# Kernel tuning notes

Measured on AMD Instinct MI355X. Metric: run time of the kernel, lower is better.

Reference implementation:

```python
import jax, jax.numpy as jnp
import numpy as np

B, C, CI, H, W = 4, 256, 128, 64, 64  # batch, in_channels, inter_channels, spatial


def conv1x1(x, w, b):
    # x: [B,C,H,W], w: [O,C], b: [O] -> [B,O,H,W]
    return jnp.einsum('bchw,oc->bohw', x, w) + b[None, :, None, None]


def setup_inputs() -> dict:
    key = jax.random.key(0)
    ks = jax.random.split(key, 9)
    s = 0.02
    return {
        'x':  jax.random.normal(ks[0], (B, C, H, W), dtype=jnp.float32),
        'Wg': jax.random.normal(ks[1], (CI, C), dtype=jnp.float32) * s,
        'bg': jnp.zeros((CI,), dtype=jnp.float32),
        'Wt': jax.random.normal(ks[2], (CI, C), dtype=jnp.float32) * s,
        'bt': jnp.zeros((CI,), dtype=jnp.float32),
        'Wp': jax.random.normal(ks[3], (CI, C), dtype=jnp.float32) * s,
        'bp': jnp.zeros((CI,), dtype=jnp.float32),
        'Wo': jax.random.normal(ks[4], (C, CI), dtype=jnp.float32) * s,
        'bo': jnp.zeros((C,), dtype=jnp.float32),
    }


def reference(x, Wg, bg, Wt, bt, Wp, bp, Wo, bo):
    b, c, h, w = x.shape
    n = h * w
    g  = conv1x1(x, Wg, bg).reshape(b, -1, n)   # [B,CI,N]
    th = conv1x1(x, Wt, bt).reshape(b, -1, n)   # [B,CI,N]
    ph = conv1x1(x, Wp, bp).reshape(b, -1, n)   # [B,CI,N]
    f = jnp.einsum('bci,bcj->bij', th, ph)      # [B,N,N] unscaled scores
    a = jax.nn.softmax(f, axis=-1)
    y = jnp.einsum('bij,bcj->bci', a, g)        # [B,CI,N]
    y = y.reshape(b, -1, h, w)
    return conv1x1(y, Wo, bo) + x
```

## Files before the change

### kernel.cpp

```cpp
#include <hip/hip_runtime.h>
#include <math.h>

#define B_  4
#define C_  256
#define CI_ 128
#define N_  4096

typedef short s16x8  __attribute__((ext_vector_type(8)));
typedef float f32x4  __attribute__((ext_vector_type(4)));
typedef float f32x16 __attribute__((ext_vector_type(16)));

__device__ inline ushort f2bf(float f) {
    unsigned int u = __float_as_uint(f);
    u += 0x7FFF + ((u >> 16) & 1);
    return (ushort)(u >> 16);
}
__device__ inline float bf2f(ushort u) {
    return __uint_as_float(((unsigned int)u) << 16);
}

__device__ inline unsigned pkbf(float a, float b) {
    unsigned r;
    asm("v_cvt_pk_bf16_f32 %0, %1, %2" : "=v"(r) : "v"(a), "v"(b));
    return r;
}
__device__ inline void plswap(unsigned &x, unsigned &y) {
    asm volatile("v_permlane32_swap_b32 %0, %1" : "+v"(x), "+v"(y));
}

__device__ inline void gload_lds16(const void* g, void* l) {
    __builtin_amdgcn_global_load_lds(
        (const __attribute__((address_space(1))) unsigned int*)g,
        (__attribute__((address_space(3))) unsigned int*)l, 16, 0, 0);
}

__device__ inline void block_sync_lds() {
    asm volatile("s_waitcnt lgkmcnt(0)" ::: "memory");
    __builtin_amdgcn_s_barrier();
    asm volatile("" ::: "memory");
}

__global__ __launch_bounds__(256) void prep_kernel(
    const float* __restrict__ Wg, const float* __restrict__ Wt,
    const float* __restrict__ Wp, const float* __restrict__ Wo,
    const float* __restrict__ bg, const float* __restrict__ bt,
    const float* __restrict__ bp,
    ushort* __restrict__ Wcat, ushort* __restrict__ Wobf,
    float* __restrict__ bcat,
    const float* __restrict__ x, ushort* __restrict__ xT)
{
    __shared__ ushort Ls[64][72];
    const int bid = blockIdx.x;
    const int t = threadIdx.x;
    if (bid < 512) {
        int i = bid * 256 + t;
        if (i < 32768)       Wcat[i] = f2bf(Wg[i]);
        else if (i < 65536)  Wcat[i] = f2bf(Wt[i - 32768]);
        else if (i < 98304)  Wcat[i] = f2bf(Wp[i - 65536]);
        else if (i < 131072) Wobf[i - 98304] = f2bf(Wo[i - 98304]);
        if (i < 128)         bcat[i] = bg[i];
        else if (i < 256)    bcat[i] = bt[i - 128];
        else if (i < 384)    bcat[i] = bp[i - 256];
        return;
    }
    int idx2 = bid - 512;
    const int n0 = (idx2 & 63) * 64;
    const int c0 = ((idx2 >> 6) & 3) * 64;
    const int b  = idx2 >> 8;
    const float* xb = x + ((size_t)b * C_ + c0) * N_ + n0;
    #pragma unroll
    for (int r = 0; r < 4; r++) {
        int idx = t + 256 * r;
        int c = idx >> 4, n4 = (idx & 15) * 4;
        float4 v = *(const float4*)&xb[(size_t)c * N_ + n4];
        ushort4 o;
        o.x = f2bf(v.x); o.y = f2bf(v.y); o.z = f2bf(v.z); o.w = f2bf(v.w);
        *(ushort4*)&Ls[c][n4] = o;
    }
    __syncthreads();
    ushort* xTb = xT + ((size_t)b * N_ + n0) * C_ + c0;
    #pragma unroll
    for (int r = 0; r < 2; r++) {
        int idx = t + 256 * r;
        int n = idx >> 3, c8 = (idx & 7) * 8;
        ushort tmp[8];
        #pragma unroll
        for (int u = 0; u < 8; u++) tmp[u] = Ls[c8 + u][n];
        *(uint4*)&xTb[(size_t)n * C_ + c8] = *(uint4*)tmp;
    }
}

__global__ __launch_bounds__(256) void proj_kernel(
    const ushort* __restrict__ Wcat, const float* __restrict__ bcat,
    const ushort* __restrict__ xT,
    ushort* __restrict__ g, ushort* __restrict__ tht, ushort* __restrict__ pht)
{
    __shared__ ushort Ws[192][72];
    __shared__ ushort Xs[64][72];
    const int b = blockIdx.z, yy = blockIdx.y, n0 = blockIdx.x * 64;
    const int t = threadIdx.x, wv = t >> 6, lane = t & 63;
    const int g4 = lane >> 4, ln = lane & 15;
    const ushort* Xsrc = xT + ((size_t)b * N_ + n0) * C_;

    f32x4 accg[4], acct[2][4];
    #pragma unroll
    for (int i = 0; i < 4; i++) {
        accg[i] = (f32x4){0.f, 0.f, 0.f, 0.f};
        acct[0][i] = (f32x4){0.f, 0.f, 0.f, 0.f};
        acct[1][i] = (f32x4){0.f, 0.f, 0.f, 0.f};
    }

    for (int k0 = 0; k0 < C_; k0 += 64) {
        block_sync_lds();
        #pragma unroll
        for (int r = 0; r < 6; r++) {
            int idx = t + 256 * r;
            int row = idx >> 3, k8 = (idx & 7) * 8;
            int srow = ((row >> 6) * 2 + yy) * 64 + (row & 63);
            *(uint4*)&Ws[row][k8] = *(const uint4*)&Wcat[(size_t)srow * C_ + k0 + k8];
        }
        #pragma unroll
        for (int r = 0; r < 2; r++) {
            int idx = t + 256 * r;
            int row = idx >> 3, k8 = (idx & 7) * 8;
            *(uint4*)&Xs[row][k8] = *(const uint4*)&Xsrc[(size_t)row * C_ + k0 + k8];
        }
        block_sync_lds();
        #pragma unroll
        for (int kk = 0; kk < 2; kk++) {
            s16x8 aW = *(const s16x8*)&Ws[16 * wv + ln][32 * kk + 8 * g4];
            #pragma unroll
            for (int nt = 0; nt < 4; nt++) {
                s16x8 bX = *(const s16x8*)&Xs[16 * nt + ln][32 * kk + 8 * g4];
                accg[nt] = __builtin_amdgcn_mfma_f32_16x16x32_bf16(aW, bX, accg[nt], 0, 0, 0);
            }
            s16x8 aX = *(const s16x8*)&Xs[16 * wv + ln][32 * kk + 8 * g4];
            #pragma unroll
            for (int mi = 0; mi < 2; mi++) {
                #pragma unroll
                for (int ct = 0; ct < 4; ct++) {
                    s16x8 bW = *(const s16x8*)&Ws[64 + 64 * mi + 16 * ct + ln][32 * kk + 8 * g4];
                    acct[mi][ct] = __builtin_amdgcn_mfma_f32_16x16x32_bf16(aX, bW, acct[mi][ct], 0, 0, 0);
                }
            }
        }
    }

    {
        ushort* ob = g + (size_t)b * CI_ * N_;
        #pragma unroll
        for (int r = 0; r < 4; r++) {
            int mloc = 16 * wv + 4 * g4 + r;
            float bi = bcat[yy * 64 + mloc];
            #pragma unroll
            for (int nt = 0; nt < 4; nt++)
                ob[(size_t)(yy * 64 + mloc) * N_ + n0 + 16 * nt + ln] = f2bf(accg[nt][r] + bi);
        }
    }
    #pragma unroll
    for (int mi = 0; mi < 2; mi++) {
        int mt = 2 + 2 * mi + yy;
        ushort* ob = (mi == 0 ? tht : pht) + (size_t)b * N_ * CI_;
        int cib = yy * 64;
        #pragma unroll
        for (int r = 0; r < 4; r++) {
            int nloc = 16 * wv + 4 * g4 + r;
            #pragma unroll
            for (int ct = 0; ct < 4; ct++) {
                float bi = bcat[mt * 64 + 16 * ct + ln];
                ob[(size_t)(n0 + nloc) * CI_ + cib + 16 * ct + ln] = f2bf(acct[mi][ct][r] + bi);
            }
        }
    }
}


__device__ inline float build_pa(const f32x16& S, s16x8& f0, s16x8& f1) {
    unsigned w[8];
    #pragma unroll
    for (int e = 0; e < 8; e++)
        w[e] = pkbf(__expf(S[2 * e]), __expf(S[2 * e + 1]));
    float ls = 0.f;
    #pragma unroll
    for (int e = 0; e < 8; e++)
        ls += __uint_as_float(w[e] << 16) + __uint_as_float(w[e] & 0xFFFF0000u);
    plswap(w[0], w[2]);
    plswap(w[1], w[3]);
    plswap(w[4], w[6]);
    plswap(w[5], w[7]);
    union { unsigned u[4]; s16x8 v; } A, B;
    A.u[0] = w[0]; A.u[1] = w[1]; A.u[2] = w[2]; A.u[3] = w[3];
    B.u[0] = w[4]; B.u[1] = w[5]; B.u[2] = w[6]; B.u[3] = w[7];
    f0 = A.v; f1 = B.v;
    return ls;
}

#define STAGE_KV(bufofs, jsrc) do {                                          \
    _Pragma("unroll")                                                        \
    for (int r_ = 0; r_ < 4; r_++) {                                         \
        int c_   = (wv << 2) + r_;                                           \
        int row_ = (c_ << 2) + kr;                                           \
        int src_ = (((jsrc) + row_) << 8) + (kc ^ ((row_ & 7) << 4));        \
        gload_lds16(kB + src_, smemB + (bufofs) + (c_ << 10));               \
    }                                                                        \
    _Pragma("unroll")                                                        \
    for (int r_ = 0; r_ < 4; r_++) {                                         \
        int c_   = (wv << 2) + r_;                                           \
        int row_ = (c_ << 3) + vr;                                           \
        int src_ = row_ * (N_ * 2) + ((jsrc) << 1) + (vc ^ ((row_ & 7) << 4));\
        gload_lds16(vB + src_, smemB + (bufofs) + 16384 + (c_ << 10));       \
    }                                                                        \
} while (0)

#define NC_ 4
#define JC_ (N_ / NC_)

__global__ __launch_bounds__(256, 2) void attn_mfma_kernel(
    const ushort* __restrict__ qn,
    const ushort* __restrict__ kn,
    const ushort* __restrict__ vm,
    ushort* __restrict__ Opart,
    float* __restrict__ lbuf)
{
    __shared__ __align__(16) char smemB[65536];

    constexpr int NI = N_ / 128;
    constexpr int nb = NI * NC_ * B_;
    int flat = (blockIdx.z * NC_ + blockIdx.y) * NI + blockIdx.x;
    int nf   = (flat & 7) * (nb / 8) + (flat >> 3);
    const int i0    = (nf % NI) * 128;
    const int chunk = (nf / NI) % NC_;
    const int b     = nf / (NI * NC_);
    const int jbase = chunk * JC_;

    const int t    = threadIdx.x;
    const int wv   = t >> 6;
    const int lane = t & 63;
    const int n32  = lane & 31;
    const int h    = lane >> 5;
    const int swz  = (n32 & 7) << 4;

    const char* kB = (const char*)(kn + (size_t)b * N_ * CI_);
    const char* vB = (const char*)(vm + (size_t)b * CI_ * N_);

    const ushort* qb = qn + ((size_t)b * N_ + i0) * CI_;
    s16x8 aQ[8];
    #pragma unroll
    for (int kk = 0; kk < 8; kk++)
        aQ[kk] = *(const s16x8*)(qb + (size_t)(32 * wv + n32) * CI_ + 16 * kk + 8 * h);

    f32x16 Oacc[4];
    #pragma unroll
    for (int dt = 0; dt < 4; dt++)
        #pragma unroll
        for (int e = 0; e < 16; e++) Oacc[dt][e] = 0.f;
    float lsum = 0.f;

    const int kr = lane >> 4;
    const int kc = (lane & 15) << 4;
    const int vr = lane >> 3;
    const int vc = (lane & 7) << 4;

    STAGE_KV(0, jbase);
    int buf = 0;
    for (int jt = jbase; jt < jbase + JC_; jt += 64) {
        if (jt + 64 < jbase + JC_) {
            STAGE_KV(buf ^ 32768, jt + 64);
            asm volatile("s_waitcnt vmcnt(8)" ::: "memory");
        } else {
            asm volatile("s_waitcnt vmcnt(0)" ::: "memory");
        }
        __builtin_amdgcn_s_barrier();
        asm volatile("" ::: "memory");

        const char* Kc = smemB + buf;
        const char* Vc = smemB + buf + 16384;

        s16x8 pa[4];
        {
            f32x16 S0;
            #pragma unroll
            for (int e = 0; e < 16; e++) S0[e] = 0.f;
            __builtin_amdgcn_s_setprio(1);
            #pragma unroll
            for (int kk = 0; kk < 8; kk++) {
                s16x8 aK = *(const s16x8*)(Kc + (n32 << 8) + (((kk << 5) + (h << 4)) ^ swz));
                S0 = __builtin_amdgcn_mfma_f32_32x32x16_bf16(aK, aQ[kk], S0, 0, 0, 0);
            }
            __builtin_amdgcn_s_setprio(0);
            lsum += build_pa(S0, pa[0], pa[1]);
        }
        {
            f32x16 S1;
            #pragma unroll
            for (int e = 0; e < 16; e++) S1[e] = 0.f;
            __builtin_amdgcn_s_setprio(1);
            #pragma unroll
            for (int kk = 0; kk < 8; kk++) {
                s16x8 aK = *(const s16x8*)(Kc + 8192 + (n32 << 8) + (((kk << 5) + (h << 4)) ^ swz));
                S1 = __builtin_amdgcn_mfma_f32_32x32x16_bf16(aK, aQ[kk], S1, 0, 0, 0);
            }
            __builtin_amdgcn_s_setprio(0);
            lsum += build_pa(S1, pa[2], pa[3]);
        }

        __builtin_amdgcn_s_setprio(1);
        #pragma unroll
        for (int dt = 0; dt < 4; dt++) {
            #pragma unroll
            for (int kk = 0; kk < 4; kk++) {
                s16x8 bV = *(const s16x8*)(Vc + ((32 * dt + n32) << 7)
                                              + (((kk << 5) + (h << 4)) ^ swz));
                Oacc[dt] = __builtin_amdgcn_mfma_f32_32x32x16_bf16(pa[kk], bV, Oacc[dt], 0, 0, 0);
            }
        }
        __builtin_amdgcn_s_setprio(0);

        block_sync_lds();
        buf ^= 32768;
    }

    ushort* Ob = Opart + (size_t)chunk * (B_ * N_ * CI_) + ((size_t)b * N_ + i0) * CI_;
    #pragma unroll
    for (int rg = 0; rg < 16; rg++) {
        int R = (rg & 3) + 8 * (rg >> 2) + 4 * h;
        int q = 32 * wv + R;
        #pragma unroll
        for (int dt = 0; dt < 4; dt++)
            Ob[(size_t)q * CI_ + 32 * dt + n32] = f2bf(Oacc[dt][rg]);
    }
    float ot  = __shfl_xor(lsum, 32);
    float tot = lsum + ot;
    if (h == 0)
        lbuf[((size_t)chunk * B_ + b) * N_ + i0 + 32 * wv + n32] = tot;
}

__global__ __launch_bounds__(256) void outgemm_kernel(
    const ushort* __restrict__ Wobf, const float* __restrict__ bo,
    const ushort* __restrict__ Opart, const float* __restrict__ lbuf,
    const float* __restrict__ x, float* __restrict__ out)
{
    __shared__ ushort Ws[64][72];
    __shared__ ushort Ys[64][72];
    const int b = blockIdx.z, m0 = blockIdx.y * 64, n0 = blockIdx.x * 64;
    const int t = threadIdx.x, wv = t >> 6, lane = t & 63;
    const int g4 = lane >> 4, ln = lane & 15;
    const ushort* Wsrc = Wobf + (size_t)m0 * CI_;
    const size_t cs = (size_t)B_ * N_ * CI_;

    f32x4 acc[4];
    #pragma unroll
    for (int i = 0; i < 4; i++) acc[i] = (f32x4){0.f, 0.f, 0.f, 0.f};

    for (int k0 = 0; k0 < CI_; k0 += 64) {
        block_sync_lds();
        #pragma unroll
        for (int r = 0; r < 2; r++) {
            int idx = t + 256 * r;
            int row = idx >> 3, k8 = (idx & 7) * 8;
            *(uint4*)&Ws[row][k8] = *(const uint4*)&Wsrc[(size_t)row * CI_ + k0 + k8];
            size_t obase = ((size_t)b * N_ + n0 + row) * CI_ + k0 + k8;
            float lsum = 0.f;
            #pragma unroll
            for (int c = 0; c < NC_; c++)
                lsum += lbuf[((size_t)c * B_ + b) * N_ + n0 + row];
            float inv = 1.0f / lsum;
            float osum[8];
            #pragma unroll
            for (int u = 0; u < 8; u++) osum[u] = 0.f;
            #pragma unroll
            for (int c = 0; c < NC_; c++) {
                ushort oc[8];
                *(uint4*)oc = *(const uint4*)&Opart[(size_t)c * cs + obase];
                #pragma unroll
                for (int u = 0; u < 8; u++) osum[u] += bf2f(oc[u]);
            }
            ushort yo[8];
            #pragma unroll
            for (int u = 0; u < 8; u++) yo[u] = f2bf(osum[u] * inv);
            *(uint4*)&Ys[row][k8] = *(uint4*)yo;
        }
        block_sync_lds();
        #pragma unroll
        for (int kk = 0; kk < 2; kk++) {
            s16x8 aW = *(const s16x8*)&Ws[16 * wv + ln][32 * kk + 8 * g4];
            #pragma unroll
            for (int nt = 0; nt < 4; nt++) {
                s16x8 bY = *(const s16x8*)&Ys[16 * nt + ln][32 * kk + 8 * g4];
                acc[nt] = __builtin_amdgcn_mfma_f32_16x16x32_bf16(aW, bY, acc[nt], 0, 0, 0);
            }
        }
    }

    float* outb = out + (size_t)b * C_ * N_;
    const float* xb = x + (size_t)b * C_ * N_;
    #pragma unroll
    for (int r = 0; r < 4; r++) {
        int m = m0 + 16 * wv + 4 * g4 + r;
        float bi = bo[m];
        #pragma unroll
        for (int nt = 0; nt < 4; nt++) {
            size_t idx = (size_t)m * N_ + n0 + 16 * nt + ln;
            outb[idx] = acc[nt][r] + bi + xb[idx];
        }
    }
}

extern "C" void kernel_launch(void* const* d_in, const int* in_sizes, int n_in,
                              void* d_out, int out_size, void* d_ws, size_t ws_size,
                              hipStream_t stream) {
    const float* x  = (const float*)d_in[0];
    const float* Wg = (const float*)d_in[1];
    const float* bg = (const float*)d_in[2];
    const float* Wt = (const float*)d_in[3];
    const float* bt = (const float*)d_in[4];
    const float* Wp = (const float*)d_in[5];
    const float* bp = (const float*)d_in[6];
    const float* Wo = (const float*)d_in[7];
    const float* bo = (const float*)d_in[8];
    float* out = (float*)d_out;

    char* w = (char*)d_ws;
    ushort* xT    = (ushort*)w;
    ushort* Opart = (ushort*)w;
    ushort* g     = (ushort*)(w + 16777216);
    ushort* tht   = (ushort*)(w + 20971520);
    ushort* pht   = (ushort*)(w + 25165824);
    ushort* Wcat  = (ushort*)(w + 29360128);
    ushort* Wobf  = (ushort*)(w + 29556736);
    float*  bcat  = (float*) (w + 29622272);
    float*  lbuf  = (float*) (w + 29623808);

    dim3 blk(256);
    prep_kernel<<<1536, blk, 0, stream>>>(Wg, Wt, Wp, Wo, bg, bt, bp,
                                          Wcat, Wobf, bcat, x, xT);
    proj_kernel<<<dim3(N_ / 64, 2, B_), blk, 0, stream>>>(Wcat, bcat, xT, g, tht, pht);
    attn_mfma_kernel<<<dim3(N_ / 128, NC_, B_), blk, 0, stream>>>(tht, pht, g, Opart, lbuf);
    outgemm_kernel<<<dim3(N_ / 64, C_ / 64, B_), blk, 0, stream>>>(Wobf, bo, Opart, lbuf, x, out);
}
```

Baseline: 150.9 us.

## Retile projection and output GEMMs to 128x128 with async LDS loads

Rewrites the projection and output 1x1-conv GEMMs to use 128x128 block tiles with 2x2 wave layout and 4x4 MFMA accumulators per wave. Operands are staged through global-to-LDS direct loads into XOR-swizzled shared memory, double-buffered in the projection kernel. The output kernel computes the softmax normalisers once per tile in shared memory. This aims to raise operand reuse and cut LDS bank conflicts and load latency, at the cost of more registers, more shared memory per block and fewer blocks in the grid.

```diff
diff --git a/kernel.cpp b/kernel.cpp
--- a/kernel.cpp
+++ b/kernel.cpp
@@ -90,90 +90,117 @@
     }
 }
 
-__global__ __launch_bounds__(256) void proj_kernel(
+__global__ __launch_bounds__(256, 2) void proj_kernel(
     const ushort* __restrict__ Wcat, const float* __restrict__ bcat,
     const ushort* __restrict__ xT,
     ushort* __restrict__ g, ushort* __restrict__ tht, ushort* __restrict__ pht)
 {
-    __shared__ ushort Ws[192][72];
-    __shared__ ushort Xs[64][72];
-    const int b = blockIdx.z, yy = blockIdx.y, n0 = blockIdx.x * 64;
+    __shared__ __align__(16) char smem[65536];
+    const int b = blockIdx.z, mt = blockIdx.y, n0 = blockIdx.x * 128;
     const int t = threadIdx.x, wv = t >> 6, lane = t & 63;
+    const int wr = wv >> 1, wc = wv & 1;
     const int g4 = lane >> 4, ln = lane & 15;
-    const ushort* Xsrc = xT + ((size_t)b * N_ + n0) * C_;
-
-    f32x4 accg[4], acct[2][4];
-    #pragma unroll
-    for (int i = 0; i < 4; i++) {
-        accg[i] = (f32x4){0.f, 0.f, 0.f, 0.f};
-        acct[0][i] = (f32x4){0.f, 0.f, 0.f, 0.f};
-        acct[1][i] = (f32x4){0.f, 0.f, 0.f, 0.f};
-    }
-
-    for (int k0 = 0; k0 < C_; k0 += 64) {
+
+    const char* Asrc = (const char*)(Wcat + (size_t)mt * 128 * C_);
+    const char* Bsrc = (const char*)(xT + ((size_t)b * N_ + n0) * C_);
+
+    const int sr = lane >> 3;
+    const int sc = (lane & 7) << 4;
+    const int ssw = sc ^ (sr << 4);
+
+    f32x4 acc[4][4];
+    #pragma unroll
+    for (int i = 0; i < 4; i++)
+        #pragma unroll
+        for (int j = 0; j < 4; j++) acc[i][j] = (f32x4){0.f, 0.f, 0.f, 0.f};
+
+    const int rsw = (ln & 7) << 4;
+
+#define PROJ_STAGE(bufofs, k0) do {                                          \
+    _Pragma("unroll")                                                        \
+    for (int r_ = 0; r_ < 4; r_++) {                                         \
+        int c_   = (wv << 2) + r_;                                           \
+        int row_ = (c_ << 3) + sr;                                           \
+        gload_lds16(Asrc + (size_t)row_ * 512 + (k0) * 2 + ssw,              \
+                    smem + (bufofs) + (c_ << 10));                           \
+        gload_lds16(Bsrc + (size_t)row_ * 512 + (k0) * 2 + ssw,              \
+                    smem + (bufofs) + 16384 + (c_ << 10));                   \
+    }                                                                        \
+} while (0)
+
+    PROJ_STAGE(0, 0);
+    int buf = 0;
+    #pragma unroll
+    for (int s = 0; s < 4; s++) {
+        if (s < 3) {
+            PROJ_STAGE(buf ^ 32768, (s + 1) * 64);
+            asm volatile("s_waitcnt vmcnt(8)" ::: "memory");
+        } else {
+            asm volatile("s_waitcnt vmcnt(0)" ::: "memory");
+        }
+        __builtin_amdgcn_s_barrier();
+        asm volatile("" ::: "memory");
+
+        const char* Ab = smem + buf;
+        const char* Bb = smem + buf + 16384;
+        #pragma unroll
+        for (int kk = 0; kk < 2; kk++) {
+            s16x8 aW[4], bX[4];
+            #pragma unroll
+            for (int m4 = 0; m4 < 4; m4++)
+                aW[m4] = *(const s16x8*)(Ab + ((wr * 64 + m4 * 16 + ln) << 7)
+                                            + (((kk << 6) + (g4 << 4)) ^ rsw));
+            #pragma unroll
+            for (int nt = 0; nt < 4; nt++)
+                bX[nt] = *(const s16x8*)(Bb + ((wc * 64 + nt * 16 + ln) << 7)
+                                            + (((kk << 6) + (g4 << 4)) ^ rsw));
+            __builtin_amdgcn_s_setprio(1);
+            #pragma unroll
+            for (int m4 = 0; m4 < 4; m4++)
+                #pragma unroll
+                for (int nt = 0; nt < 4; nt++)
+                    acc[m4][nt] = __builtin_amdgcn_mfma_f32_16x16x32_bf16(
+                        aW[m4], bX[nt], acc[m4][nt], 0, 0, 0);
+            __builtin_amdgcn_s_setprio(0);
+        }
         block_sync_lds();
-        #pragma unroll
-        for (int r = 0; r < 6; r++) {
-            int idx = t + 256 * r;
-            int row = idx >> 3, k8 = (idx & 7) * 8;
-            int srow = ((row >> 6) * 2 + yy) * 64 + (row & 63);
-            *(uint4*)&Ws[row][k8] = *(const uint4*)&Wcat[(size_t)srow * C_ + k0 + k8];
-        }
-        #pragma unroll
-        for (int r = 0; r < 2; r++) {
-            int idx = t + 256 * r;
-            int row = idx >> 3, k8 = (idx & 7) * 8;
-            *(uint4*)&Xs[row][k8] = *(const uint4*)&Xsrc[(size_t)row * C_ + k0 + k8];
-        }
-        block_sync_lds();
-        #pragma unroll
-        for (int kk = 0; kk < 2; kk++) {
-            s16x8 aW = *(const s16x8*)&Ws[16 * wv + ln][32 * kk + 8 * g4];
+        buf ^= 32768;
+    }
+
+    if (mt == 0) {
+        ushort* ob = g + (size_t)b * CI_ * N_;
+        #pragma unroll
+        for (int m4 = 0; m4 < 4; m4++) {
+            #pragma unroll
+            for (int r = 0; r < 4; r++) {
+                int m = wr * 64 + m4 * 16 + 4 * g4 + r;
+                float bi = bcat[m];
+                #pragma unroll
+                for (int nt = 0; nt < 4; nt++) {
+                    int n = n0 + wc * 64 + nt * 16 + ln;
+                    ob[(size_t)m * N_ + n] = f2bf(acc[m4][nt][r] + bi);
+                }
+            }
+        }
+    } else {
+        ushort* ob = (mt == 1 ? tht : pht) + (size_t)b * N_ * CI_;
+        const float* bb = bcat + mt * 128;
+        #pragma unroll
+        for (int m4 = 0; m4 < 4; m4++) {
+            int mbase = wr * 64 + m4 * 16 + 4 * g4;
             #pragma unroll
             for (int nt = 0; nt < 4; nt++) {
-                s16x8 bX = *(const s16x8*)&Xs[16 * nt + ln][32 * kk + 8 * g4];
-                accg[nt] = __builtin_amdgcn_mfma_f32_16x16x32_bf16(aW, bX, accg[nt], 0, 0, 0);
-            }
-            s16x8 aX = *(const s16x8*)&Xs[16 * wv + ln][32 * kk + 8 * g4];
-            #pragma unroll
-            for (int mi = 0; mi < 2; mi++) {
+                int n = n0 + wc * 64 + nt * 16 + ln;
+                ushort v4[4];
                 #pragma unroll
-                for (int ct = 0; ct < 4; ct++) {
-                    s16x8 bW = *(const s16x8*)&Ws[64 + 64 * mi + 16 * ct + ln][32 * kk + 8 * g4];
-                    acct[mi][ct] = __builtin_amdgcn_mfma_f32_16x16x32_bf16(aX, bW, acct[mi][ct], 0, 0, 0);
-                }
-            }
-        }
-    }
-
-    {
-        ushort* ob = g + (size_t)b * CI_ * N_;
-        #pragma unroll
-        for (int r = 0; r < 4; r++) {
-            int mloc = 16 * wv + 4 * g4 + r;
-            float bi = bcat[yy * 64 + mloc];
-            #pragma unroll
-            for (int nt = 0; nt < 4; nt++)
-                ob[(size_t)(yy * 64 + mloc) * N_ + n0 + 16 * nt + ln] = f2bf(accg[nt][r] + bi);
-        }
-    }
-    #pragma unroll
-    for (int mi = 0; mi < 2; mi++) {
-        int mt = 2 + 2 * mi + yy;
-        ushort* ob = (mi == 0 ? tht : pht) + (size_t)b * N_ * CI_;
-        int cib = yy * 64;
-        #pragma unroll
-        for (int r = 0; r < 4; r++) {
-            int nloc = 16 * wv + 4 * g4 + r;
-            #pragma unroll
-            for (int ct = 0; ct < 4; ct++) {
-                float bi = bcat[mt * 64 + 16 * ct + ln];
-                ob[(size_t)(n0 + nloc) * CI_ + cib + 16 * ct + ln] = f2bf(acct[mi][ct][r] + bi);
-            }
-        }
-    }
-}
-
+                for (int r = 0; r < 4; r++)
+                    v4[r] = f2bf(acc[m4][nt][r] + bb[mbase + r]);
+                *(ushort4*)&ob[(size_t)n * CI_ + mbase] = *(ushort4*)v4;
+            }
+        }
+    }
+#undef PROJ_STAGE
+}
 
 __device__ inline float build_pa(const f32x16& S, s16x8& f0, s16x8& f1) {
     unsigned w[8];
@@ -335,73 +362,109 @@
         lbuf[((size_t)chunk * B_ + b) * N_ + i0 + 32 * wv + n32] = tot;
 }
 
-__global__ __launch_bounds__(256) void outgemm_kernel(
+__global__ __launch_bounds__(256, 2) void outgemm_kernel(
     const ushort* __restrict__ Wobf, const float* __restrict__ bo,
     const ushort* __restrict__ Opart, const float* __restrict__ lbuf,
     const float* __restrict__ x, float* __restrict__ out)
 {
-    __shared__ ushort Ws[64][72];
-    __shared__ ushort Ys[64][72];
-    const int b = blockIdx.z, m0 = blockIdx.y * 64, n0 = blockIdx.x * 64;
+    __shared__ __align__(16) char smem[65536];
+    __shared__ float invL[128];
+    const int b = blockIdx.z, m0 = blockIdx.y * 128, n0 = blockIdx.x * 128;
     const int t = threadIdx.x, wv = t >> 6, lane = t & 63;
+    const int wr = wv >> 1, wc = wv & 1;
     const int g4 = lane >> 4, ln = lane & 15;
-    const ushort* Wsrc = Wobf + (size_t)m0 * CI_;
     const size_t cs = (size_t)B_ * N_ * CI_;
 
-    f32x4 acc[4];
-    #pragma unroll
-    for (int i = 0; i < 4; i++) acc[i] = (f32x4){0.f, 0.f, 0.f, 0.f};
-
-    for (int k0 = 0; k0 < CI_; k0 += 64) {
-        block_sync_lds();
-        #pragma unroll
-        for (int r = 0; r < 2; r++) {
-            int idx = t + 256 * r;
-            int row = idx >> 3, k8 = (idx & 7) * 8;
-            *(uint4*)&Ws[row][k8] = *(const uint4*)&Wsrc[(size_t)row * CI_ + k0 + k8];
-            size_t obase = ((size_t)b * N_ + n0 + row) * CI_ + k0 + k8;
-            float lsum = 0.f;
-            #pragma unroll
-            for (int c = 0; c < NC_; c++)
-                lsum += lbuf[((size_t)c * B_ + b) * N_ + n0 + row];
-            float inv = 1.0f / lsum;
+    {
+        const char* Wsrc = (const char*)(Wobf + (size_t)m0 * CI_);
+        int srl = lane >> 4;
+        int scl = (lane & 15) << 4;
+        #pragma unroll
+        for (int r = 0; r < 8; r++) {
+            int c   = (wv << 3) + r;
+            int row = (c << 2) + srl;
+            gload_lds16(Wsrc + (size_t)row * 256 + (scl ^ ((row & 15) << 4)),
+                        smem + (c << 10));
+        }
+    }
+
+    if (t < 128) {
+        float ls = 0.f;
+        #pragma unroll
+        for (int c = 0; c < NC_; c++)
+            ls += lbuf[((size_t)c * B_ + b) * N_ + n0 + t];
+        invL[t] = 1.0f / ls;
+    }
+    block_sync_lds();
+
+    {
+        #pragma unroll
+        for (int r = 0; r < 8; r++) {
+            int c   = t + 256 * r;
+            int row = c >> 4;
+            int col = (c & 15) << 4;
+            size_t obase = ((size_t)b * N_ + n0 + row) * CI_ + (c & 15) * 8;
+            float inv = invL[row];
             float osum[8];
             #pragma unroll
             for (int u = 0; u < 8; u++) osum[u] = 0.f;
             #pragma unroll
-            for (int c = 0; c < NC_; c++) {
+            for (int cc = 0; cc < NC_; cc++) {
                 ushort oc[8];
-                *(uint4*)oc = *(const uint4*)&Opart[(size_t)c * cs + obase];
+                *(uint4*)oc = *(const uint4*)&Opart[(size_t)cc * cs + obase];
                 #pragma unroll
                 for (int u = 0; u < 8; u++) osum[u] += bf2f(oc[u]);
             }
             ushort yo[8];
             #pragma unroll
             for (int u = 0; u < 8; u++) yo[u] = f2bf(osum[u] * inv);
-            *(uint4*)&Ys[row][k8] = *(uint4*)yo;
-        }
-        block_sync_lds();
-        #pragma unroll
-        for (int kk = 0; kk < 2; kk++) {
-            s16x8 aW = *(const s16x8*)&Ws[16 * wv + ln][32 * kk + 8 * g4];
-            #pragma unroll
-            for (int nt = 0; nt < 4; nt++) {
-                s16x8 bY = *(const s16x8*)&Ys[16 * nt + ln][32 * kk + 8 * g4];
-                acc[nt] = __builtin_amdgcn_mfma_f32_16x16x32_bf16(aW, bY, acc[nt], 0, 0, 0);
-            }
-        }
+            *(uint4*)(smem + 32768 + row * 256 + (col ^ ((row & 15) << 4))) = *(uint4*)yo;
+        }
+    }
+    asm volatile("s_waitcnt vmcnt(0)" ::: "memory");
+    block_sync_lds();
+
+    f32x4 acc[4][4];
+    #pragma unroll
+    for (int i = 0; i < 4; i++)
+        #pragma unroll
+        for (int j = 0; j < 4; j++) acc[i][j] = (f32x4){0.f, 0.f, 0.f, 0.f};
+
+    const int rsw = ln << 4;
+    #pragma unroll
+    for (int kk = 0; kk < 4; kk++) {
+        s16x8 aW[4], bY[4];
+        #pragma unroll
+        for (int m4 = 0; m4 < 4; m4++)
+            aW[m4] = *(const s16x8*)(smem + ((wr * 64 + m4 * 16 + ln) << 8)
+                                          + (((kk << 6) + (g4 << 4)) ^ rsw));
+        #pragma unroll
+        for (int nt = 0; nt < 4; nt++)
+            bY[nt] = *(const s16x8*)(smem + 32768 + ((wc * 64 + nt * 16 + ln) << 8)
+                                          + (((kk << 6) + (g4 << 4)) ^ rsw));
+        __builtin_amdgcn_s_setprio(1);
+        #pragma unroll
+        for (int m4 = 0; m4 < 4; m4++)
+            #pragma unroll
+            for (int nt = 0; nt < 4; nt++)
+                acc[m4][nt] = __builtin_amdgcn_mfma_f32_16x16x32_bf16(
+                    aW[m4], bY[nt], acc[m4][nt], 0, 0, 0);
+        __builtin_amdgcn_s_setprio(0);
     }
 
     float* outb = out + (size_t)b * C_ * N_;
     const float* xb = x + (size_t)b * C_ * N_;
     #pragma unroll
-    for (int r = 0; r < 4; r++) {
-        int m = m0 + 16 * wv + 4 * g4 + r;
-        float bi = bo[m];
-        #pragma unroll
-        for (int nt = 0; nt < 4; nt++) {
-            size_t idx = (size_t)m * N_ + n0 + 16 * nt + ln;
-            outb[idx] = acc[nt][r] + bi + xb[idx];
+    for (int m4 = 0; m4 < 4; m4++) {
+        #pragma unroll
+        for (int r = 0; r < 4; r++) {
+            int m = m0 + wr * 64 + m4 * 16 + 4 * g4 + r;
+            float bi = bo[m];
+            #pragma unroll
+            for (int nt = 0; nt < 4; nt++) {
+                size_t idx = (size_t)m * N_ + n0 + wc * 64 + nt * 16 + ln;
+                outb[idx] = acc[m4][nt][r] + bi + xb[idx];
+            }
         }
     }
 }
@@ -434,7 +497,7 @@
     dim3 blk(256);
     prep_kernel<<<1536, blk, 0, stream>>>(Wg, Wt, Wp, Wo, bg, bt, bp,
                                           Wcat, Wobf, bcat, x, xT);
-    proj_kernel<<<dim3(N_ / 64, 2, B_), blk, 0, stream>>>(Wcat, bcat, xT, g, tht, pht);
+    proj_kernel<<<dim3(N_ / 128, 3, B_), blk, 0, stream>>>(Wcat, bcat, xT, g, tht, pht);
     attn_mfma_kernel<<<dim3(N_ / 128, NC_, B_), blk, 0, stream>>>(tht, pht, g, Opart, lbuf);
-    outgemm_kernel<<<dim3(N_ / 64, C_ / 64, B_), blk, 0, stream>>>(Wobf, bo, Opart, lbuf, x, out);
-}
+    outgemm_kernel<<<dim3(N_ / 128, C_ / 128, B_), blk, 0, stream>>>(Wobf, bo, Opart, lbuf, x, out);
+}
```

New measurement: 145.4 us. 3.6% less time.
